# Kernel optimization log

Measured on AMD Instinct MI355X. Metric: run time of the kernel, lower is better.

The kernel has to match this reference:

```python
import jax, jax.numpy as jnp
import numpy as np

HIDDEN = 1024
INTER = 4096
NUM_EXPERTS = 8
TOP_K = 2
BATCH, SEQ = 2, 1024


def setup_inputs() -> dict:
    key = jax.random.key(0)
    ks = jax.random.split(key, 5)
    s_h = 1.0 / np.sqrt(HIDDEN)
    s_f = 1.0 / np.sqrt(INTER)
    x = jax.random.normal(ks[0], (BATCH, SEQ, HIDDEN), dtype=jnp.float32)
    gate_w = jax.random.normal(ks[1], (HIDDEN, NUM_EXPERTS), dtype=jnp.float32) * s_h
    w_gate = jax.random.normal(ks[2], (NUM_EXPERTS, HIDDEN, INTER), dtype=jnp.float32) * s_h
    w_up = jax.random.normal(ks[3], (NUM_EXPERTS, HIDDEN, INTER), dtype=jnp.float32) * s_h
    w_down = jax.random.normal(ks[4], (NUM_EXPERTS, INTER, HIDDEN), dtype=jnp.float32) * s_f
    return {"x": x, "gate_w": gate_w, "w_gate": w_gate, "w_up": w_up, "w_down": w_down}


def reference(x, gate_w, w_gate, w_up, w_down):
    B, S, H = x.shape
    E = w_gate.shape[0]
    xf = x.reshape(-1, H)  # [T, H]

    # Router: softmax over experts, take top-k, then re-softmax the top-k PROBS
    # (the torch module applies softmax to the probabilities, not the logits).
    gate_probs = jax.nn.softmax(xf @ gate_w, axis=-1)          # [T, E]
    topk_p, topk_i = jax.lax.top_k(gate_probs, TOP_K)           # [T, K]
    topk_w = jax.nn.softmax(topk_p, axis=-1)                    # [T, K]

    # Combine weights per (token, expert): sum of topk weights routed to e.
    combine = jnp.einsum('tke,tk->te', jax.nn.one_hot(topk_i, E, dtype=xf.dtype), topk_w)  # [T, E]

    # Dense all-expert SwiGLU MLP, then weighted combine (same math as masked loop).
    g = jax.nn.silu(jnp.einsum('th,ehf->etf', xf, w_gate))      # [E, T, F]
    u = jnp.einsum('th,ehf->etf', xf, w_up)                     # [E, T, F]
    d = jnp.einsum('etf,efh->eth', g * u, w_down)               # [E, T, H]
    out = jnp.einsum('eth,te->th', d, combine)                  # [T, H]
    return out.reshape(B, S, H)
```

## Files before the change

### kernel.cpp

```cpp
#include <hip/hip_runtime.h>
#include <hip/hip_bf16.h>
#include <cstdint>


typedef short short8 __attribute__((ext_vector_type(8)));
typedef float floatx4 __attribute__((ext_vector_type(4)));

#define H_DIM 1024
#define F_DIM 4096
#define N_EXP 8
#define T_TOK 2048
#define MCAP  5120

#define BM 128
#define BN 64
#define BK 32
#define LDT 40

struct Meta {
  int cnt[N_EXP];
  int cursor[N_EXP];
  int poff[N_EXP + 1];
  int pad0;
  int pair_token[MCAP];
  float pair_w[MCAP];
  int token_pair[2 * T_TOK];
  int tok_e[2 * T_TOK];
  float tok_w[2 * T_TOK];
};

__device__ __forceinline__ unsigned short f2b(float f) {
  unsigned int u = __float_as_uint(f);
  u = (u + 0x7fffu + ((u >> 16) & 1u)) >> 16;
  return (unsigned short)u;
}
__device__ __forceinline__ float b2f(unsigned short h) {
  return __uint_as_float(((unsigned int)h) << 16);
}

__global__ void k_init(Meta* __restrict__ m) {
  int i = threadIdx.x;
  if (i < N_EXP) { m->cnt[i] = 0; m->cursor[i] = 0; }
}

__global__ __launch_bounds__(64)
void k_router(const float* __restrict__ x, const float* __restrict__ gw,
              Meta* __restrict__ m) {
  int t = blockIdx.x;
  int lane = threadIdx.x;
  const float* xr = x + (size_t)t * H_DIM;
  float acc[N_EXP];
#pragma unroll
  for (int e = 0; e < N_EXP; ++e) acc[e] = 0.f;
  for (int i = 0; i < H_DIM / 64; ++i) {
    int h = i * 64 + lane;
    float xv = xr[h];
    const float* g = gw + (size_t)h * N_EXP;
#pragma unroll
    for (int e = 0; e < N_EXP; ++e) acc[e] += xv * g[e];
  }
#pragma unroll
  for (int e = 0; e < N_EXP; ++e) {
    float v = acc[e];
    for (int off = 32; off; off >>= 1) v += __shfl_xor(v, off, 64);
    acc[e] = v;
  }
  if (lane == 0) {
    float mx = acc[0];
    for (int e = 1; e < N_EXP; ++e) mx = fmaxf(mx, acc[e]);
    float p[N_EXP];
    float s = 0.f;
    for (int e = 0; e < N_EXP; ++e) { p[e] = __expf(acc[e] - mx); s += p[e]; }
    float inv = 1.f / s;
    for (int e = 0; e < N_EXP; ++e) p[e] *= inv;
    int i1 = 0;
    for (int e = 1; e < N_EXP; ++e) if (p[e] > p[i1]) i1 = e;
    int i2 = (i1 == 0) ? 1 : 0;
    for (int e = 0; e < N_EXP; ++e) if (e != i1 && p[e] > p[i2]) i2 = e;
    float w1 = 1.f / (1.f + __expf(p[i2] - p[i1]));
    m->tok_e[2 * t] = i1;     m->tok_e[2 * t + 1] = i2;
    m->tok_w[2 * t] = w1;     m->tok_w[2 * t + 1] = 1.f - w1;
    atomicAdd(&m->cnt[i1], 1);
    atomicAdd(&m->cnt[i2], 1);
  }
}

__global__ void k_scan(Meta* __restrict__ m) {
  if (threadIdx.x == 0 && blockIdx.x == 0) {
    int o = 0;
    for (int e = 0; e < N_EXP; ++e) {
      m->poff[e] = o;
      o += ((m->cnt[e] + BM - 1) / BM) * BM;
    }
    m->poff[N_EXP] = o;
  }
}

__global__ void k_assign(Meta* __restrict__ m) {
  int t = blockIdx.x * blockDim.x + threadIdx.x;
  if (t >= T_TOK) return;
  for (int k = 0; k < 2; ++k) {
    int e = m->tok_e[2 * t + k];
    int idx = atomicAdd(&m->cursor[e], 1);
    int p = m->poff[e] + idx;
    m->pair_token[p] = t;
    m->pair_w[p] = m->tok_w[2 * t + k];
    m->token_pair[2 * t + k] = p;
  }
}

__global__ __launch_bounds__(256)
void k_gather(const float* __restrict__ x, unsigned short* __restrict__ Xe,
              const Meta* __restrict__ m) {
  int r = blockIdx.x;
  if (r >= m->poff[N_EXP]) return;
  int e = 0;
#pragma unroll
  for (int i = 1; i < N_EXP; ++i) if (r >= m->poff[i]) e = i;
  bool real = (r - m->poff[e]) < m->cnt[e];
  int h = threadIdx.x * 4;
  ushort4 sv = {0, 0, 0, 0};
  if (real) {
    int t = m->pair_token[r];
    float4 f = *(const float4*)(x + (size_t)t * H_DIM + h);
    sv.x = f2b(f.x); sv.y = f2b(f.y); sv.z = f2b(f.z); sv.w = f2b(f.w);
  }
  *(ushort4*)(Xe + (size_t)r * H_DIM + h) = sv;
}

__global__ __launch_bounds__(256, 2)
void k_gemm_dual(const unsigned short* __restrict__ Xe,
                 const float* __restrict__ w_gate,
                 const float* __restrict__ w_up,
                 unsigned short* __restrict__ Aw,
                 const Meta* __restrict__ m) {
  __shared__ unsigned short As[BM * LDT];
  __shared__ unsigned short Bg[BN * LDT];
  __shared__ unsigned short Bu[BN * LDT];
  int tileM = blockIdx.y * BM;
  if (tileM >= m->poff[N_EXP]) return;
  int e = 0;
#pragma unroll
  for (int i = 1; i < N_EXP; ++i) if (tileM >= m->poff[i]) e = i;
  int n0 = blockIdx.x * BN;
  const float* Wg = w_gate + (size_t)e * H_DIM * F_DIM;
  const float* Wu = w_up   + (size_t)e * H_DIM * F_DIM;

  int tid = threadIdx.x;
  int lane = tid & 63;
  int wid = tid >> 6;
  int wm = (wid & 1) * 64;
  int wn = (wid >> 1) * 32;
  int lm = lane & 15;
  int quad = lane >> 4;

  floatx4 accG[4][2] = {};
  floatx4 accU[4][2] = {};

  for (int k0 = 0; k0 < H_DIM; k0 += BK) {
    {
      int c = tid;
#pragma unroll
      for (int it = 0; it < 2; ++it, c += 256) {
        int row = c >> 2, kp = c & 3;
        *(uint4*)&As[row * LDT + kp * 8] =
            *(const uint4*)(Xe + (size_t)(tileM + row) * H_DIM + k0 + kp * 8);
      }
    }
    {
      int nn = tid & 63;
      int kh = tid >> 6;
      const float* sg = Wg + (size_t)(k0 + kh * 8) * F_DIM + n0 + nn;
      const float* su = Wu + (size_t)(k0 + kh * 8) * F_DIM + n0 + nn;
      short8 vg, vu;
#pragma unroll
      for (int j = 0; j < 8; ++j) {
        vg[j] = (short)f2b(sg[(size_t)j * F_DIM]);
        vu[j] = (short)f2b(su[(size_t)j * F_DIM]);
      }
      *(short8*)&Bg[nn * LDT + kh * 8] = vg;
      *(short8*)&Bu[nn * LDT + kh * 8] = vu;
    }
    __syncthreads();
    short8 a[4];
#pragma unroll
    for (int fm = 0; fm < 4; ++fm)
      a[fm] = *(const short8*)&As[(wm + fm * 16 + lm) * LDT + quad * 8];
#pragma unroll
    for (int fn = 0; fn < 2; ++fn) {
      short8 bg = *(const short8*)&Bg[(wn + fn * 16 + lm) * LDT + quad * 8];
      short8 bu = *(const short8*)&Bu[(wn + fn * 16 + lm) * LDT + quad * 8];
#pragma unroll
      for (int fm = 0; fm < 4; ++fm) {
        accG[fm][fn] = __builtin_amdgcn_mfma_f32_16x16x32_bf16(a[fm], bg, accG[fm][fn], 0, 0, 0);
        accU[fm][fn] = __builtin_amdgcn_mfma_f32_16x16x32_bf16(a[fm], bu, accU[fm][fn], 0, 0, 0);
      }
    }
    __syncthreads();
  }
#pragma unroll
  for (int fm = 0; fm < 4; ++fm)
#pragma unroll
    for (int fn = 0; fn < 2; ++fn)
#pragma unroll
      for (int r = 0; r < 4; ++r) {
        int row = tileM + wm + fm * 16 + quad * 4 + r;
        int col = n0 + wn + fn * 16 + lm;
        float g = accG[fm][fn][r];
        float u = accU[fm][fn][r];
        float s = g / (1.f + __expf(-g));
        Aw[(size_t)row * F_DIM + col] = f2b(s * u);
      }
}

__global__ __launch_bounds__(256, 2)
void k_gemm_down(const unsigned short* __restrict__ Aw,
                 const float* __restrict__ w_down,
                 unsigned short* __restrict__ Y,
                 const Meta* __restrict__ m) {
  __shared__ unsigned short As[BM * LDT];
  __shared__ unsigned short Bs[BN * LDT];
  int tileM = blockIdx.y * BM;
  if (tileM >= m->poff[N_EXP]) return;
  int e = 0;
#pragma unroll
  for (int i = 1; i < N_EXP; ++i) if (tileM >= m->poff[i]) e = i;
  int n0 = blockIdx.x * BN;
  const float* W = w_down + (size_t)e * F_DIM * H_DIM;

  int tid = threadIdx.x;
  int lane = tid & 63;
  int wid = tid >> 6;
  int wm = (wid & 1) * 64;
  int wn = (wid >> 1) * 32;
  int lm = lane & 15;
  int quad = lane >> 4;

  floatx4 acc[4][2] = {};

  for (int k0 = 0; k0 < F_DIM; k0 += BK) {
    {
      int c = tid;
#pragma unroll
      for (int it = 0; it < 2; ++it, c += 256) {
        int row = c >> 2, kp = c & 3;
        *(uint4*)&As[row * LDT + kp * 8] =
            *(const uint4*)(Aw + (size_t)(tileM + row) * F_DIM + k0 + kp * 8);
      }
    }
    {
      int nn = tid & 63;
      int kh = tid >> 6;
      const float* s = W + (size_t)(k0 + kh * 8) * H_DIM + n0 + nn;
      short8 v;
#pragma unroll
      for (int j = 0; j < 8; ++j) v[j] = (short)f2b(s[(size_t)j * H_DIM]);
      *(short8*)&Bs[nn * LDT + kh * 8] = v;
    }
    __syncthreads();
    short8 a[4];
#pragma unroll
    for (int fm = 0; fm < 4; ++fm)
      a[fm] = *(const short8*)&As[(wm + fm * 16 + lm) * LDT + quad * 8];
#pragma unroll
    for (int fn = 0; fn < 2; ++fn) {
      short8 b = *(const short8*)&Bs[(wn + fn * 16 + lm) * LDT + quad * 8];
#pragma unroll
      for (int fm = 0; fm < 4; ++fm)
        acc[fm][fn] = __builtin_amdgcn_mfma_f32_16x16x32_bf16(a[fm], b, acc[fm][fn], 0, 0, 0);
    }
    __syncthreads();
  }
#pragma unroll
  for (int fm = 0; fm < 4; ++fm)
#pragma unroll
    for (int fn = 0; fn < 2; ++fn)
#pragma unroll
      for (int r = 0; r < 4; ++r) {
        int row = tileM + wm + fm * 16 + quad * 4 + r;
        int col = n0 + wn + fn * 16 + lm;
        Y[(size_t)row * H_DIM + col] = f2b(acc[fm][fn][r]);
      }
}

__global__ __launch_bounds__(256)
void k_combine(const unsigned short* __restrict__ Y, const Meta* __restrict__ m,
               float* __restrict__ out) {
  int t = blockIdx.x;
  int h = threadIdx.x * 4;
  int p0 = m->token_pair[2 * t];
  int p1 = m->token_pair[2 * t + 1];
  float w0 = m->pair_w[p0];
  float w1 = m->pair_w[p1];
  ushort4 y0 = *(const ushort4*)(Y + (size_t)p0 * H_DIM + h);
  ushort4 y1 = *(const ushort4*)(Y + (size_t)p1 * H_DIM + h);
  float4 o;
  o.x = w0 * b2f(y0.x) + w1 * b2f(y1.x);
  o.y = w0 * b2f(y0.y) + w1 * b2f(y1.y);
  o.z = w0 * b2f(y0.z) + w1 * b2f(y1.z);
  o.w = w0 * b2f(y0.w) + w1 * b2f(y1.w);
  *(float4*)(out + (size_t)t * H_DIM + h) = o;
}

extern "C" void kernel_launch(void* const* d_in, const int* in_sizes, int n_in,
                              void* d_out, int out_size, void* d_ws, size_t ws_size,
                              hipStream_t stream) {
  const float* x  = (const float*)d_in[0];
  const float* gw = (const float*)d_in[1];
  const float* wg = (const float*)d_in[2];
  const float* wu = (const float*)d_in[3];
  const float* wd = (const float*)d_in[4];
  float* out = (float*)d_out;

  unsigned short* Xe = (unsigned short*)d_ws;
  unsigned short* Aw = Xe + (size_t)MCAP * H_DIM;
  unsigned short* Y  = Aw + (size_t)MCAP * F_DIM;
  Meta* m = (Meta*)(Y + (size_t)MCAP * H_DIM);

  k_init<<<1, 64, 0, stream>>>(m);
  k_router<<<T_TOK, 64, 0, stream>>>(x, gw, m);
  k_scan<<<1, 64, 0, stream>>>(m);
  k_assign<<<T_TOK / 256, 256, 0, stream>>>(m);
  k_gather<<<MCAP, 256, 0, stream>>>(x, Xe, m);
  k_gemm_dual<<<dim3(F_DIM / BN, MCAP / BM), 256, 0, stream>>>(Xe, wg, wu, Aw, m);
  k_gemm_down<<<dim3(H_DIM / BN, MCAP / BM), 256, 0, stream>>>(Aw, wd, Y, m);
  k_combine<<<T_TOK, 256, 0, stream>>>(Y, m, out);
}
```

Baseline: 628.2 us.

## Pre-convert expert weights to tiled bf16 and load tiles via global_load_lds

Adds a prep kernel that converts the fp32 expert weights each call into a bf16, k-major tiled layout in workspace. The GEMMs then fetch A and B tiles with direct global-to-LDS 16-byte loads, replacing strided fp32 scalar loads and per-element conversion in the inner loop. The cost is an extra full pass over about 400MB of fp32 weights plus about 200MB of bf16 writes on every call. A fallback path keeps the old kernels when the workspace is too small.

```diff
diff --git a/kernel.cpp b/kernel.cpp
--- a/kernel.cpp
+++ b/kernel.cpp
@@ -36,6 +36,12 @@
 }
 __device__ __forceinline__ float b2f(unsigned short h) {
   return __uint_as_float(((unsigned int)h) << 16);
+}
+
+__device__ __forceinline__ void gll16(const void* g, void* l) {
+  __builtin_amdgcn_global_load_lds(
+      (const __attribute__((address_space(1))) unsigned int*)g,
+      (__attribute__((address_space(3))) unsigned int*)l, 16, 0, 0);
 }
 
 __global__ void k_init(Meta* __restrict__ m) {
@@ -128,23 +134,53 @@
   *(ushort4*)(Xe + (size_t)r * H_DIM + h) = sv;
 }
 
+__global__ __launch_bounds__(256)
+void k_prep(const float* __restrict__ W, unsigned short* __restrict__ Wt,
+            int K, int NT, int N) {
+  __shared__ __align__(16) unsigned short Ls[2048];
+  int e = blockIdx.y, nt = blockIdx.x;
+  int t = threadIdx.x;
+  int KB = K >> 5;
+  int kb0 = blockIdx.z * 32;
+  int kb1 = kb0 + 32;
+  int k = t >> 3;
+  int nc = (t & 7) * 8;
+  for (int kb = kb0; kb < kb1; ++kb) {
+    const float* src = W + ((size_t)e * K + (size_t)kb * 32 + k) * N + (size_t)nt * 64 + nc;
+    float4 f0 = *(const float4*)src;
+    float4 f1 = *(const float4*)(src + 4);
+    Ls[(nc + 0) * 32 + k] = f2b(f0.x);
+    Ls[(nc + 1) * 32 + k] = f2b(f0.y);
+    Ls[(nc + 2) * 32 + k] = f2b(f0.z);
+    Ls[(nc + 3) * 32 + k] = f2b(f0.w);
+    Ls[(nc + 4) * 32 + k] = f2b(f1.x);
+    Ls[(nc + 5) * 32 + k] = f2b(f1.y);
+    Ls[(nc + 6) * 32 + k] = f2b(f1.z);
+    Ls[(nc + 7) * 32 + k] = f2b(f1.w);
+    __syncthreads();
+    short8 v = *(const short8*)&Ls[t * 8];
+    size_t dst = (((size_t)e * NT + nt) * KB + kb) * 2048 + (size_t)t * 8;
+    *(short8*)&Wt[dst] = v;
+    __syncthreads();
+  }
+}
+
 __global__ __launch_bounds__(256, 2)
-void k_gemm_dual(const unsigned short* __restrict__ Xe,
-                 const float* __restrict__ w_gate,
-                 const float* __restrict__ w_up,
-                 unsigned short* __restrict__ Aw,
-                 const Meta* __restrict__ m) {
-  __shared__ unsigned short As[BM * LDT];
-  __shared__ unsigned short Bg[BN * LDT];
-  __shared__ unsigned short Bu[BN * LDT];
+void k_gemm_dual2(const unsigned short* __restrict__ Xe,
+                  const unsigned short* __restrict__ WtG,
+                  const unsigned short* __restrict__ WtU,
+                  unsigned short* __restrict__ Aw,
+                  const Meta* __restrict__ m) {
+  __shared__ __align__(16) unsigned short As[BM * 32];
+  __shared__ __align__(16) unsigned short Bg[BN * 32];
+  __shared__ __align__(16) unsigned short Bu[BN * 32];
   int tileM = blockIdx.y * BM;
   if (tileM >= m->poff[N_EXP]) return;
   int e = 0;
 #pragma unroll
   for (int i = 1; i < N_EXP; ++i) if (tileM >= m->poff[i]) e = i;
-  int n0 = blockIdx.x * BN;
-  const float* Wg = w_gate + (size_t)e * H_DIM * F_DIM;
-  const float* Wu = w_up   + (size_t)e * H_DIM * F_DIM;
+  int nt = blockIdx.x;
+  int n0 = nt * BN;
 
   int tid = threadIdx.x;
   int lane = tid & 63;
@@ -157,39 +193,26 @@
   floatx4 accG[4][2] = {};
   floatx4 accU[4][2] = {};
 
+  int c0 = wid * 128 + lane;
+  int c1 = c0 + 64;
+  int bc = wid * 64 + lane;
+
   for (int k0 = 0; k0 < H_DIM; k0 += BK) {
-    {
-      int c = tid;
-#pragma unroll
-      for (int it = 0; it < 2; ++it, c += 256) {
-        int row = c >> 2, kp = c & 3;
-        *(uint4*)&As[row * LDT + kp * 8] =
-            *(const uint4*)(Xe + (size_t)(tileM + row) * H_DIM + k0 + kp * 8);
-      }
-    }
-    {
-      int nn = tid & 63;
-      int kh = tid >> 6;
-      const float* sg = Wg + (size_t)(k0 + kh * 8) * F_DIM + n0 + nn;
-      const float* su = Wu + (size_t)(k0 + kh * 8) * F_DIM + n0 + nn;
-      short8 vg, vu;
-#pragma unroll
-      for (int j = 0; j < 8; ++j) {
-        vg[j] = (short)f2b(sg[(size_t)j * F_DIM]);
-        vu[j] = (short)f2b(su[(size_t)j * F_DIM]);
-      }
-      *(short8*)&Bg[nn * LDT + kh * 8] = vg;
-      *(short8*)&Bu[nn * LDT + kh * 8] = vu;
-    }
+    int kb = k0 >> 5;
+    size_t btile = (((size_t)e * (F_DIM / 64) + nt) * (H_DIM / 32) + kb) * 2048;
+    gll16(Xe + (size_t)(tileM + (c0 >> 2)) * H_DIM + k0 + (c0 & 3) * 8, &As[wid * 1024]);
+    gll16(Xe + (size_t)(tileM + (c1 >> 2)) * H_DIM + k0 + (c1 & 3) * 8, &As[wid * 1024 + 512]);
+    gll16(WtG + btile + (size_t)bc * 8, &Bg[wid * 512]);
+    gll16(WtU + btile + (size_t)bc * 8, &Bu[wid * 512]);
     __syncthreads();
     short8 a[4];
 #pragma unroll
     for (int fm = 0; fm < 4; ++fm)
-      a[fm] = *(const short8*)&As[(wm + fm * 16 + lm) * LDT + quad * 8];
+      a[fm] = *(const short8*)&As[(wm + fm * 16 + lm) * 32 + quad * 8];
 #pragma unroll
     for (int fn = 0; fn < 2; ++fn) {
-      short8 bg = *(const short8*)&Bg[(wn + fn * 16 + lm) * LDT + quad * 8];
-      short8 bu = *(const short8*)&Bu[(wn + fn * 16 + lm) * LDT + quad * 8];
+      short8 bg = *(const short8*)&Bg[(wn + fn * 16 + lm) * 32 + quad * 8];
+      short8 bu = *(const short8*)&Bu[(wn + fn * 16 + lm) * 32 + quad * 8];
 #pragma unroll
       for (int fm = 0; fm < 4; ++fm) {
         accG[fm][fn] = __builtin_amdgcn_mfma_f32_16x16x32_bf16(a[fm], bg, accG[fm][fn], 0, 0, 0);
@@ -214,19 +237,19 @@
 }
 
 __global__ __launch_bounds__(256, 2)
-void k_gemm_down(const unsigned short* __restrict__ Aw,
-                 const float* __restrict__ w_down,
-                 unsigned short* __restrict__ Y,
-                 const Meta* __restrict__ m) {
-  __shared__ unsigned short As[BM * LDT];
-  __shared__ unsigned short Bs[BN * LDT];
+void k_gemm_down2(const unsigned short* __restrict__ Aw,
+                  const unsigned short* __restrict__ WtD,
+                  unsigned short* __restrict__ Y,
+                  const Meta* __restrict__ m) {
+  __shared__ __align__(16) unsigned short As[BM * 32];
+  __shared__ __align__(16) unsigned short Bs[BN * 32];
   int tileM = blockIdx.y * BM;
   if (tileM >= m->poff[N_EXP]) return;
   int e = 0;
 #pragma unroll
   for (int i = 1; i < N_EXP; ++i) if (tileM >= m->poff[i]) e = i;
-  int n0 = blockIdx.x * BN;
-  const float* W = w_down + (size_t)e * F_DIM * H_DIM;
+  int nt = blockIdx.x;
+  int n0 = nt * BN;
 
   int tid = threadIdx.x;
   int lane = tid & 63;
@@ -238,6 +261,146 @@
 
   floatx4 acc[4][2] = {};
 
+  int c0 = wid * 128 + lane;
+  int c1 = c0 + 64;
+  int bc = wid * 64 + lane;
+
+  for (int k0 = 0; k0 < F_DIM; k0 += BK) {
+    int kb = k0 >> 5;
+    size_t btile = (((size_t)e * (H_DIM / 64) + nt) * (F_DIM / 32) + kb) * 2048;
+    gll16(Aw + (size_t)(tileM + (c0 >> 2)) * F_DIM + k0 + (c0 & 3) * 8, &As[wid * 1024]);
+    gll16(Aw + (size_t)(tileM + (c1 >> 2)) * F_DIM + k0 + (c1 & 3) * 8, &As[wid * 1024 + 512]);
+    gll16(WtD + btile + (size_t)bc * 8, &Bs[wid * 512]);
+    __syncthreads();
+    short8 a[4];
+#pragma unroll
+    for (int fm = 0; fm < 4; ++fm)
+      a[fm] = *(const short8*)&As[(wm + fm * 16 + lm) * 32 + quad * 8];
+#pragma unroll
+    for (int fn = 0; fn < 2; ++fn) {
+      short8 b = *(const short8*)&Bs[(wn + fn * 16 + lm) * 32 + quad * 8];
+#pragma unroll
+      for (int fm = 0; fm < 4; ++fm)
+        acc[fm][fn] = __builtin_amdgcn_mfma_f32_16x16x32_bf16(a[fm], b, acc[fm][fn], 0, 0, 0);
+    }
+    __syncthreads();
+  }
+#pragma unroll
+  for (int fm = 0; fm < 4; ++fm)
+#pragma unroll
+    for (int fn = 0; fn < 2; ++fn)
+#pragma unroll
+      for (int r = 0; r < 4; ++r) {
+        int row = tileM + wm + fm * 16 + quad * 4 + r;
+        int col = n0 + wn + fn * 16 + lm;
+        Y[(size_t)row * H_DIM + col] = f2b(acc[fm][fn][r]);
+      }
+}
+
+__global__ __launch_bounds__(256, 2)
+void k_gemm_dual_fb(const unsigned short* __restrict__ Xe,
+                    const float* __restrict__ w_gate,
+                    const float* __restrict__ w_up,
+                    unsigned short* __restrict__ Aw,
+                    const Meta* __restrict__ m) {
+  __shared__ unsigned short As[BM * LDT];
+  __shared__ unsigned short Bg[BN * LDT];
+  __shared__ unsigned short Bu[BN * LDT];
+  int tileM = blockIdx.y * BM;
+  if (tileM >= m->poff[N_EXP]) return;
+  int e = 0;
+#pragma unroll
+  for (int i = 1; i < N_EXP; ++i) if (tileM >= m->poff[i]) e = i;
+  int n0 = blockIdx.x * BN;
+  const float* Wg = w_gate + (size_t)e * H_DIM * F_DIM;
+  const float* Wu = w_up   + (size_t)e * H_DIM * F_DIM;
+  int tid = threadIdx.x;
+  int lane = tid & 63;
+  int wid = tid >> 6;
+  int wm = (wid & 1) * 64;
+  int wn = (wid >> 1) * 32;
+  int lm = lane & 15;
+  int quad = lane >> 4;
+  floatx4 accG[4][2] = {};
+  floatx4 accU[4][2] = {};
+  for (int k0 = 0; k0 < H_DIM; k0 += BK) {
+    {
+      int c = tid;
+#pragma unroll
+      for (int it = 0; it < 2; ++it, c += 256) {
+        int row = c >> 2, kp = c & 3;
+        *(uint4*)&As[row * LDT + kp * 8] =
+            *(const uint4*)(Xe + (size_t)(tileM + row) * H_DIM + k0 + kp * 8);
+      }
+    }
+    {
+      int nn = tid & 63;
+      int kh = tid >> 6;
+      const float* sg = Wg + (size_t)(k0 + kh * 8) * F_DIM + n0 + nn;
+      const float* su = Wu + (size_t)(k0 + kh * 8) * F_DIM + n0 + nn;
+      short8 vg, vu;
+#pragma unroll
+      for (int j = 0; j < 8; ++j) {
+        vg[j] = (short)f2b(sg[(size_t)j * F_DIM]);
+        vu[j] = (short)f2b(su[(size_t)j * F_DIM]);
+      }
+      *(short8*)&Bg[nn * LDT + kh * 8] = vg;
+      *(short8*)&Bu[nn * LDT + kh * 8] = vu;
+    }
+    __syncthreads();
+    short8 a[4];
+#pragma unroll
+    for (int fm = 0; fm < 4; ++fm)
+      a[fm] = *(const short8*)&As[(wm + fm * 16 + lm) * LDT + quad * 8];
+#pragma unroll
+    for (int fn = 0; fn < 2; ++fn) {
+      short8 bg = *(const short8*)&Bg[(wn + fn * 16 + lm) * LDT + quad * 8];
+      short8 bu = *(const short8*)&Bu[(wn + fn * 16 + lm) * LDT + quad * 8];
+#pragma unroll
+      for (int fm = 0; fm < 4; ++fm) {
+        accG[fm][fn] = __builtin_amdgcn_mfma_f32_16x16x32_bf16(a[fm], bg, accG[fm][fn], 0, 0, 0);
+        accU[fm][fn] = __builtin_amdgcn_mfma_f32_16x16x32_bf16(a[fm], bu, accU[fm][fn], 0, 0, 0);
+      }
+    }
+    __syncthreads();
+  }
+#pragma unroll
+  for (int fm = 0; fm < 4; ++fm)
+#pragma unroll
+    for (int fn = 0; fn < 2; ++fn)
+#pragma unroll
+      for (int r = 0; r < 4; ++r) {
+        int row = tileM + wm + fm * 16 + quad * 4 + r;
+        int col = n0 + wn + fn * 16 + lm;
+        float g = accG[fm][fn][r];
+        float u = accU[fm][fn][r];
+        float s = g / (1.f + __expf(-g));
+        Aw[(size_t)row * F_DIM + col] = f2b(s * u);
+      }
+}
+
+__global__ __launch_bounds__(256, 2)
+void k_gemm_down_fb(const unsigned short* __restrict__ Aw,
+                    const float* __restrict__ w_down,
+                    unsigned short* __restrict__ Y,
+                    const Meta* __restrict__ m) {
+  __shared__ unsigned short As[BM * LDT];
+  __shared__ unsigned short Bs[BN * LDT];
+  int tileM = blockIdx.y * BM;
+  if (tileM >= m->poff[N_EXP]) return;
+  int e = 0;
+#pragma unroll
+  for (int i = 1; i < N_EXP; ++i) if (tileM >= m->poff[i]) e = i;
+  int n0 = blockIdx.x * BN;
+  const float* W = w_down + (size_t)e * F_DIM * H_DIM;
+  int tid = threadIdx.x;
+  int lane = tid & 63;
+  int wid = tid >> 6;
+  int wm = (wid & 1) * 64;
+  int wn = (wid >> 1) * 32;
+  int lm = lane & 15;
+  int quad = lane >> 4;
+  floatx4 acc[4][2] = {};
   for (int k0 = 0; k0 < F_DIM; k0 += BK) {
     {
       int c = tid;
@@ -316,13 +479,29 @@
   unsigned short* Aw = Xe + (size_t)MCAP * H_DIM;
   unsigned short* Y  = Aw + (size_t)MCAP * F_DIM;
   Meta* m = (Meta*)(Y + (size_t)MCAP * H_DIM);
+  uintptr_t wtp = ((uintptr_t)(m + 1) + 255) & ~(uintptr_t)255;
+  unsigned short* WtG = (unsigned short*)wtp;
+  const size_t WSZ = (size_t)N_EXP * H_DIM * F_DIM;
+  unsigned short* WtU = WtG + WSZ;
+  unsigned short* WtD = WtU + WSZ;
+  size_t need = (size_t)((char*)(WtD + WSZ) - (char*)d_ws);
+  bool big = ws_size >= need;
 
   k_init<<<1, 64, 0, stream>>>(m);
   k_router<<<T_TOK, 64, 0, stream>>>(x, gw, m);
   k_scan<<<1, 64, 0, stream>>>(m);
   k_assign<<<T_TOK / 256, 256, 0, stream>>>(m);
   k_gather<<<MCAP, 256, 0, stream>>>(x, Xe, m);
-  k_gemm_dual<<<dim3(F_DIM / BN, MCAP / BM), 256, 0, stream>>>(Xe, wg, wu, Aw, m);
-  k_gemm_down<<<dim3(H_DIM / BN, MCAP / BM), 256, 0, stream>>>(Aw, wd, Y, m);
+
+  if (big) {
+    k_prep<<<dim3(F_DIM / 64, N_EXP, 1), 256, 0, stream>>>(wg, WtG, H_DIM, F_DIM / 64, F_DIM);
+    k_prep<<<dim3(F_DIM / 64, N_EXP, 1), 256, 0, stream>>>(wu, WtU, H_DIM, F_DIM / 64, F_DIM);
+    k_prep<<<dim3(H_DIM / 64, N_EXP, 4), 256, 0, stream>>>(wd, WtD, F_DIM, H_DIM / 64, H_DIM);
+    k_gemm_dual2<<<dim3(F_DIM / BN, MCAP / BM), 256, 0, stream>>>(Xe, WtG, WtU, Aw, m);
+    k_gemm_down2<<<dim3(H_DIM / BN, MCAP / BM), 256, 0, stream>>>(Aw, WtD, Y, m);
+  } else {
+    k_gemm_dual_fb<<<dim3(F_DIM / BN, MCAP / BM), 256, 0, stream>>>(Xe, wg, wu, Aw, m);
+    k_gemm_down_fb<<<dim3(H_DIM / BN, MCAP / BM), 256, 0, stream>>>(Aw, wd, Y, m);
+  }
   k_combine<<<T_TOK, 256, 0, stream>>>(Y, m, out);
 }
```

Result: slower. 699.0 us (+11.3%).

## Pre-convert weights to tiled bf16 and load GEMM tiles directly into LDS

Applied to the files above, without the earlier changes.

Adds per-call prep kernels that convert gate, up and down weights from fp32 into a bf16 layout tiled to match the GEMM blocks. The GEMMs then stage A and B tiles with global_load_lds 16-byte loads instead of strided fp32 reads with in-loop conversion, and drop the LDS padding. The router now packs four tokens per block and reads the gate weights as vectors. A single-block plan kernel replaces the init, scan and assign kernels. The trade-off is an extra full pass that reads and writes all weights each call, plus extra workspace, and the unpadded LDS layout may cause bank conflicts.

```diff
diff --git a/kernel.cpp b/kernel.cpp
--- a/kernel.cpp
+++ b/kernel.cpp
@@ -15,13 +15,10 @@
 #define BM 128
 #define BN 64
 #define BK 32
-#define LDT 40
 
 struct Meta {
   int cnt[N_EXP];
-  int cursor[N_EXP];
   int poff[N_EXP + 1];
-  int pad0;
   int pair_token[MCAP];
   float pair_w[MCAP];
   int token_pair[2 * T_TOK];
@@ -38,26 +35,32 @@
   return __uint_as_float(((unsigned int)h) << 16);
 }
 
-__global__ void k_init(Meta* __restrict__ m) {
-  int i = threadIdx.x;
-  if (i < N_EXP) { m->cnt[i] = 0; m->cursor[i] = 0; }
-}
-
-__global__ __launch_bounds__(64)
+__device__ __forceinline__ void gll16(const void* g, void* l) {
+  __builtin_amdgcn_global_load_lds(
+      (const __attribute__((address_space(1))) unsigned int*)g,
+      (__attribute__((address_space(3))) unsigned int*)l, 16, 0, 0);
+}
+
+__global__ __launch_bounds__(256)
 void k_router(const float* __restrict__ x, const float* __restrict__ gw,
               Meta* __restrict__ m) {
-  int t = blockIdx.x;
-  int lane = threadIdx.x;
+  int wave = threadIdx.x >> 6, lane = threadIdx.x & 63;
+  int t = blockIdx.x * 4 + wave;
   const float* xr = x + (size_t)t * H_DIM;
   float acc[N_EXP];
 #pragma unroll
   for (int e = 0; e < N_EXP; ++e) acc[e] = 0.f;
+#pragma unroll 4
   for (int i = 0; i < H_DIM / 64; ++i) {
     int h = i * 64 + lane;
     float xv = xr[h];
     const float* g = gw + (size_t)h * N_EXP;
-#pragma unroll
-    for (int e = 0; e < N_EXP; ++e) acc[e] += xv * g[e];
+    float4 g0 = *(const float4*)g;
+    float4 g1 = *(const float4*)(g + 4);
+    acc[0] += xv * g0.x; acc[1] += xv * g0.y;
+    acc[2] += xv * g0.z; acc[3] += xv * g0.w;
+    acc[4] += xv * g1.x; acc[5] += xv * g1.y;
+    acc[6] += xv * g1.z; acc[7] += xv * g1.w;
   }
 #pragma unroll
   for (int e = 0; e < N_EXP; ++e) {
@@ -80,32 +83,33 @@
     float w1 = 1.f / (1.f + __expf(p[i2] - p[i1]));
     m->tok_e[2 * t] = i1;     m->tok_e[2 * t + 1] = i2;
     m->tok_w[2 * t] = w1;     m->tok_w[2 * t + 1] = 1.f - w1;
-    atomicAdd(&m->cnt[i1], 1);
-    atomicAdd(&m->cnt[i2], 1);
-  }
-}
-
-__global__ void k_scan(Meta* __restrict__ m) {
-  if (threadIdx.x == 0 && blockIdx.x == 0) {
+  }
+}
+
+__global__ __launch_bounds__(256)
+void k_plan(Meta* __restrict__ m) {
+  __shared__ int hist[N_EXP], cur[N_EXP], off[N_EXP + 1];
+  int t = threadIdx.x;
+  if (t < N_EXP) { hist[t] = 0; cur[t] = 0; }
+  __syncthreads();
+  for (int i = t; i < 2 * T_TOK; i += 256) atomicAdd(&hist[m->tok_e[i]], 1);
+  __syncthreads();
+  if (t == 0) {
     int o = 0;
     for (int e = 0; e < N_EXP; ++e) {
-      m->poff[e] = o;
-      o += ((m->cnt[e] + BM - 1) / BM) * BM;
+      off[e] = o; m->poff[e] = o; m->cnt[e] = hist[e];
+      o += ((hist[e] + BM - 1) / BM) * BM;
     }
-    m->poff[N_EXP] = o;
-  }
-}
-
-__global__ void k_assign(Meta* __restrict__ m) {
-  int t = blockIdx.x * blockDim.x + threadIdx.x;
-  if (t >= T_TOK) return;
-  for (int k = 0; k < 2; ++k) {
-    int e = m->tok_e[2 * t + k];
-    int idx = atomicAdd(&m->cursor[e], 1);
-    int p = m->poff[e] + idx;
-    m->pair_token[p] = t;
-    m->pair_w[p] = m->tok_w[2 * t + k];
-    m->token_pair[2 * t + k] = p;
+    off[N_EXP] = o; m->poff[N_EXP] = o;
+  }
+  __syncthreads();
+  for (int i = t; i < 2 * T_TOK; i += 256) {
+    int e = m->tok_e[i];
+    int idx = atomicAdd(&cur[e], 1);
+    int p = off[e] + idx;
+    m->pair_token[p] = i >> 1;
+    m->pair_w[p] = m->tok_w[i];
+    m->token_pair[i] = p;
   }
 }
 
@@ -128,23 +132,76 @@
   *(ushort4*)(Xe + (size_t)r * H_DIM + h) = sv;
 }
 
-__global__ __launch_bounds__(256, 2)
-void k_gemm_dual(const unsigned short* __restrict__ Xe,
-                 const float* __restrict__ w_gate,
-                 const float* __restrict__ w_up,
-                 unsigned short* __restrict__ Aw,
-                 const Meta* __restrict__ m) {
-  __shared__ unsigned short As[BM * LDT];
-  __shared__ unsigned short Bg[BN * LDT];
-  __shared__ unsigned short Bu[BN * LDT];
+__global__ __launch_bounds__(256, 4)
+void k_prep_gu(const float* __restrict__ wg, const float* __restrict__ wu,
+               unsigned short* __restrict__ WtG, unsigned short* __restrict__ WtU) {
+  const int K = H_DIM, N = F_DIM, NT = F_DIM / 64, KB = K >> 5;
+  int zi = blockIdx.z;
+  const float* W = (zi < 8) ? wg : wu;
+  unsigned short* Wt = (zi < 8) ? WtG : WtU;
+  int e = blockIdx.y, nt = blockIdx.x;
+  int t = threadIdx.x;
+  int wid = t >> 6, lane = t & 63;
+  int dn = lane >> 2, k8 = lane & 3;
+  int n = wid * 16 + dn;
+  int kb0 = (zi & 7) * 4;
+#pragma unroll
+  for (int i = 0; i < 4; ++i) {
+    int kb = kb0 + i;
+    const float* src = W + ((size_t)e * K + (size_t)kb * 32 + k8 * 8) * N
+                         + (size_t)nt * 64 + n;
+    float v[8];
+#pragma unroll
+    for (int j = 0; j < 8; ++j) v[j] = src[(size_t)j * N];
+    short8 o;
+#pragma unroll
+    for (int j = 0; j < 8; ++j) o[j] = (short)f2b(v[j]);
+    size_t dst = (((size_t)e * NT + nt) * KB + kb) * 2048 + (size_t)t * 8;
+    *(short8*)&Wt[dst] = o;
+  }
+}
+
+__global__ __launch_bounds__(256, 4)
+void k_prep_d(const float* __restrict__ W, unsigned short* __restrict__ Wt) {
+  const int K = F_DIM, N = H_DIM, NT = H_DIM / 64, KB = K >> 5;
+  int e = blockIdx.y, nt = blockIdx.x;
+  int t = threadIdx.x;
+  int wid = t >> 6, lane = t & 63;
+  int dn = lane >> 2, k8 = lane & 3;
+  int n = wid * 16 + dn;
+  int kb0 = blockIdx.z * 4;
+#pragma unroll
+  for (int i = 0; i < 4; ++i) {
+    int kb = kb0 + i;
+    const float* src = W + ((size_t)e * K + (size_t)kb * 32 + k8 * 8) * N
+                         + (size_t)nt * 64 + n;
+    float v[8];
+#pragma unroll
+    for (int j = 0; j < 8; ++j) v[j] = src[(size_t)j * N];
+    short8 o;
+#pragma unroll
+    for (int j = 0; j < 8; ++j) o[j] = (short)f2b(v[j]);
+    size_t dst = (((size_t)e * NT + nt) * KB + kb) * 2048 + (size_t)t * 8;
+    *(short8*)&Wt[dst] = o;
+  }
+}
+
+__global__ __launch_bounds__(256, 4)
+void k_gemm_dual2(const unsigned short* __restrict__ Xe,
+                  const unsigned short* __restrict__ WtG,
+                  const unsigned short* __restrict__ WtU,
+                  unsigned short* __restrict__ Aw,
+                  const Meta* __restrict__ m) {
+  __shared__ __align__(16) unsigned short As[BM * 32];
+  __shared__ __align__(16) unsigned short Bg[BN * 32];
+  __shared__ __align__(16) unsigned short Bu[BN * 32];
   int tileM = blockIdx.y * BM;
   if (tileM >= m->poff[N_EXP]) return;
   int e = 0;
 #pragma unroll
   for (int i = 1; i < N_EXP; ++i) if (tileM >= m->poff[i]) e = i;
-  int n0 = blockIdx.x * BN;
-  const float* Wg = w_gate + (size_t)e * H_DIM * F_DIM;
-  const float* Wu = w_up   + (size_t)e * H_DIM * F_DIM;
+  int nt = blockIdx.x;
+  int n0 = nt * BN;
 
   int tid = threadIdx.x;
   int lane = tid & 63;
@@ -157,39 +214,26 @@
   floatx4 accG[4][2] = {};
   floatx4 accU[4][2] = {};
 
+  int c0 = wid * 128 + lane;
+  int c1 = c0 + 64;
+  int bc = wid * 64 + lane;
+
   for (int k0 = 0; k0 < H_DIM; k0 += BK) {
-    {
-      int c = tid;
-#pragma unroll
-      for (int it = 0; it < 2; ++it, c += 256) {
-        int row = c >> 2, kp = c & 3;
-        *(uint4*)&As[row * LDT + kp * 8] =
-            *(const uint4*)(Xe + (size_t)(tileM + row) * H_DIM + k0 + kp * 8);
-      }
-    }
-    {
-      int nn = tid & 63;
-      int kh = tid >> 6;
-      const float* sg = Wg + (size_t)(k0 + kh * 8) * F_DIM + n0 + nn;
-      const float* su = Wu + (size_t)(k0 + kh * 8) * F_DIM + n0 + nn;
-      short8 vg, vu;
-#pragma unroll
-      for (int j = 0; j < 8; ++j) {
-        vg[j] = (short)f2b(sg[(size_t)j * F_DIM]);
-        vu[j] = (short)f2b(su[(size_t)j * F_DIM]);
-      }
-      *(short8*)&Bg[nn * LDT + kh * 8] = vg;
-      *(short8*)&Bu[nn * LDT + kh * 8] = vu;
-    }
+    int kb = k0 >> 5;
+    size_t btile = (((size_t)e * (F_DIM / 64) + nt) * (H_DIM / 32) + kb) * 2048;
+    gll16(Xe + (size_t)(tileM + (c0 >> 2)) * H_DIM + k0 + (c0 & 3) * 8, &As[wid * 1024]);
+    gll16(Xe + (size_t)(tileM + (c1 >> 2)) * H_DIM + k0 + (c1 & 3) * 8, &As[wid * 1024 + 512]);
+    gll16(WtG + btile + (size_t)bc * 8, &Bg[wid * 512]);
+    gll16(WtU + btile + (size_t)bc * 8, &Bu[wid * 512]);
     __syncthreads();
     short8 a[4];
 #pragma unroll
     for (int fm = 0; fm < 4; ++fm)
-      a[fm] = *(const short8*)&As[(wm + fm * 16 + lm) * LDT + quad * 8];
+      a[fm] = *(const short8*)&As[(wm + fm * 16 + lm) * 32 + quad * 8];
 #pragma unroll
     for (int fn = 0; fn < 2; ++fn) {
-      short8 bg = *(const short8*)&Bg[(wn + fn * 16 + lm) * LDT + quad * 8];
-      short8 bu = *(const short8*)&Bu[(wn + fn * 16 + lm) * LDT + quad * 8];
+      short8 bg = *(const short8*)&Bg[(wn + fn * 16 + lm) * 32 + quad * 8];
+      short8 bu = *(const short8*)&Bu[(wn + fn * 16 + lm) * 32 + quad * 8];
 #pragma unroll
       for (int fm = 0; fm < 4; ++fm) {
         accG[fm][fn] = __builtin_amdgcn_mfma_f32_16x16x32_bf16(a[fm], bg, accG[fm][fn], 0, 0, 0);
@@ -213,20 +257,20 @@
       }
 }
 
-__global__ __launch_bounds__(256, 2)
-void k_gemm_down(const unsigned short* __restrict__ Aw,
-                 const float* __restrict__ w_down,
-                 unsigned short* __restrict__ Y,
-                 const Meta* __restrict__ m) {
-  __shared__ unsigned short As[BM * LDT];
-  __shared__ unsigned short Bs[BN * LDT];
+__global__ __launch_bounds__(256, 4)
+void k_gemm_down2(const unsigned short* __restrict__ Aw,
+                  const unsigned short* __restrict__ WtD,
+                  unsigned short* __restrict__ Y,
+                  const Meta* __restrict__ m) {
+  __shared__ __align__(16) unsigned short As[BM * 32];
+  __shared__ __align__(16) unsigned short Bs[BN * 32];
   int tileM = blockIdx.y * BM;
   if (tileM >= m->poff[N_EXP]) return;
   int e = 0;
 #pragma unroll
   for (int i = 1; i < N_EXP; ++i) if (tileM >= m->poff[i]) e = i;
-  int n0 = blockIdx.x * BN;
-  const float* W = w_down + (size_t)e * F_DIM * H_DIM;
+  int nt = blockIdx.x;
+  int n0 = nt * BN;
 
   int tid = threadIdx.x;
   int lane = tid & 63;
@@ -238,33 +282,24 @@
 
   floatx4 acc[4][2] = {};
 
+  int c0 = wid * 128 + lane;
+  int c1 = c0 + 64;
+  int bc = wid * 64 + lane;
+
   for (int k0 = 0; k0 < F_DIM; k0 += BK) {
-    {
-      int c = tid;
-#pragma unroll
-      for (int it = 0; it < 2; ++it, c += 256) {
-        int row = c >> 2, kp = c & 3;
-        *(uint4*)&As[row * LDT + kp * 8] =
-            *(const uint4*)(Aw + (size_t)(tileM + row) * F_DIM + k0 + kp * 8);
-      }
-    }
-    {
-      int nn = tid & 63;
-      int kh = tid >> 6;
-      const float* s = W + (size_t)(k0 + kh * 8) * H_DIM + n0 + nn;
-      short8 v;
-#pragma unroll
-      for (int j = 0; j < 8; ++j) v[j] = (short)f2b(s[(size_t)j * H_DIM]);
-      *(short8*)&Bs[nn * LDT + kh * 8] = v;
-    }
+    int kb = k0 >> 5;
+    size_t btile = (((size_t)e * (H_DIM / 64) + nt) * (F_DIM / 32) + kb) * 2048;
+    gll16(Aw + (size_t)(tileM + (c0 >> 2)) * F_DIM + k0 + (c0 & 3) * 8, &As[wid * 1024]);
+    gll16(Aw + (size_t)(tileM + (c1 >> 2)) * F_DIM + k0 + (c1 & 3) * 8, &As[wid * 1024 + 512]);
+    gll16(WtD + btile + (size_t)bc * 8, &Bs[wid * 512]);
     __syncthreads();
     short8 a[4];
 #pragma unroll
     for (int fm = 0; fm < 4; ++fm)
-      a[fm] = *(const short8*)&As[(wm + fm * 16 + lm) * LDT + quad * 8];
+      a[fm] = *(const short8*)&As[(wm + fm * 16 + lm) * 32 + quad * 8];
 #pragma unroll
     for (int fn = 0; fn < 2; ++fn) {
-      short8 b = *(const short8*)&Bs[(wn + fn * 16 + lm) * LDT + quad * 8];
+      short8 b = *(const short8*)&Bs[(wn + fn * 16 + lm) * 32 + quad * 8];
 #pragma unroll
       for (int fm = 0; fm < 4; ++fm)
         acc[fm][fn] = __builtin_amdgcn_mfma_f32_16x16x32_bf16(a[fm], b, acc[fm][fn], 0, 0, 0);
@@ -316,13 +351,18 @@
   unsigned short* Aw = Xe + (size_t)MCAP * H_DIM;
   unsigned short* Y  = Aw + (size_t)MCAP * F_DIM;
   Meta* m = (Meta*)(Y + (size_t)MCAP * H_DIM);
-
-  k_init<<<1, 64, 0, stream>>>(m);
-  k_router<<<T_TOK, 64, 0, stream>>>(x, gw, m);
-  k_scan<<<1, 64, 0, stream>>>(m);
-  k_assign<<<T_TOK / 256, 256, 0, stream>>>(m);
+  uintptr_t wtp = ((uintptr_t)(m + 1) + 255) & ~(uintptr_t)255;
+  unsigned short* WtG = (unsigned short*)wtp;
+  const size_t WSZ = (size_t)N_EXP * H_DIM * F_DIM;
+  unsigned short* WtU = WtG + WSZ;
+  unsigned short* WtD = WtU + WSZ;
+
+  k_router<<<T_TOK / 4, 256, 0, stream>>>(x, gw, m);
+  k_plan<<<1, 256, 0, stream>>>(m);
   k_gather<<<MCAP, 256, 0, stream>>>(x, Xe, m);
-  k_gemm_dual<<<dim3(F_DIM / BN, MCAP / BM), 256, 0, stream>>>(Xe, wg, wu, Aw, m);
-  k_gemm_down<<<dim3(H_DIM / BN, MCAP / BM), 256, 0, stream>>>(Aw, wd, Y, m);
+  k_prep_gu<<<dim3(F_DIM / 64, N_EXP, 16), 256, 0, stream>>>(wg, wu, WtG, WtU);
+  k_prep_d<<<dim3(H_DIM / 64, N_EXP, 32), 256, 0, stream>>>(wd, WtD);
+  k_gemm_dual2<<<dim3(F_DIM / BN, MCAP / BM), 256, 0, stream>>>(Xe, WtG, WtU, Aw, m);
+  k_gemm_down2<<<dim3(H_DIM / BN, MCAP / BM), 256, 0, stream>>>(Aw, WtD, Y, m);
   k_combine<<<T_TOK, 256, 0, stream>>>(Y, m, out);
 }
```

Measured after the change: 629.5 us. No clear change (+0.2%).
